# Kernel tuning notes

Hardware: AMD Instinct MI355X
Metric: run time of the kernel (lower is better)

Reference implementation:

```python
import jax, jax.numpy as jnp
import numpy as np

B, T, C = 4, 768, 2048
HEAD_SIZE = 64
H = C // HEAD_SIZE
D_W, D_A, D_MV, D_G = 96, 96, 64, 256
GN_EPS = 1e-5 * 8 ** 2  # head_size_divisor = 8


def _layer_norm(x, w, b, eps=1e-5):
    m = jnp.mean(x, -1, keepdims=True)
    v = jnp.mean(jnp.square(x - m), -1, keepdims=True)
    return (x - m) * jax.lax.rsqrt(v + eps) * w + b


def _time_shift(x):
    # ZeroPad2d((0,0,1,-1)): prepend a zero timestep, drop the last
    return jnp.pad(x, ((0, 0), (1, 0), (0, 0)))[:, :-1]


def _group_norm(x, w, b, eps):
    # x: [M, C], H groups
    M, Cc = x.shape
    xg = x.reshape(M, H, Cc // H)
    m = jnp.mean(xg, -1, keepdims=True)
    v = jnp.mean(jnp.square(xg - m), -1, keepdims=True)
    xg = (xg - m) * jax.lax.rsqrt(v + eps)
    return xg.reshape(M, Cc) * w + b


def _rwkv7(r, w, k, v, a, b):
    # WindBackstepping semantics: S_t = S_{t-1} * diag(exp(-exp(w_t))) + S_{t-1} a_t b_t^T + v_t k_t^T
    # y_t = S_t r_t ; state S is [B,H,N(v),N(k)]
    Bb, Tt, Cc = r.shape
    N = HEAD_SIZE
    r, w, k, v, a, b = [t.reshape(Bb, Tt, H, N) for t in (r, w, k, v, a, b)]
    decay = jnp.exp(-jnp.exp(w))  # [B,T,H,N]
    seq = tuple(jnp.moveaxis(t, 1, 0) for t in (decay, r, k, v, a, b))  # [T,B,H,N]
    s0 = jnp.zeros((Bb, H, N, N), jnp.float32)

    def step(s, inp):
        d_t, r_t, k_t, v_t, a_t, b_t = inp
        sab = jnp.einsum('bhik,bhk,bhj->bhij', s, a_t, b_t)
        s = s * d_t[:, :, None, :] + sab + v_t[..., :, None] * k_t[..., None, :]
        y_t = jnp.einsum('bhij,bhj->bhi', s, r_t)
        return s, y_t

    _, y = jax.lax.scan(step, s0, seq)
    return jnp.moveaxis(y, 0, 1).reshape(Bb, Tt, Cc)


def setup_inputs() -> dict:
    key = jax.random.key(0)
    ks = iter(jax.random.split(key, 48))
    rn = lambda shape, s=1.0: jax.random.normal(next(ks), shape, jnp.float32) * s
    d = {}
    d['x'] = rn((B, T, C))
    d['v_first'] = rn((B, T, C))
    d['ln1_w'] = jnp.ones((C,)); d['ln1_b'] = jnp.zeros((C,))
    d['ln2_w'] = jnp.ones((C,)); d['ln2_b'] = jnp.zeros((C,))
    ddd = jnp.arange(C, dtype=jnp.float32) / C
    for nm, p in [('x_r', 0.2), ('x_w', 0.9), ('x_k', 0.9), ('x_v', 0.4), ('x_a', 0.9), ('x_g', 0.2)]:
        d[nm] = 1.0 - jnp.power(ddd, p)
    d['w0'] = jnp.linspace(-7.0, -2.0, C) + 0.5
    d['w1'] = rn((C, D_W), 0.01); d['w2'] = rn((D_W, C), 0.02)
    d['a0'] = rn((C,), 0.1); d['a1'] = rn((C, D_A), 0.01); d['a2'] = rn((D_A, C), 0.02)
    d['v0'] = 1.0 + rn((C,), 0.1); d['v1'] = rn((C, D_MV), 0.01); d['v2'] = rn((D_MV, C), 0.02)
    d['g1'] = rn((C, D_G), 0.01); d['g2'] = rn((D_G, C), 0.02)
    d['k_k'] = 0.85 * jnp.ones((C,)); d['k_a'] = jnp.ones((C,))
    d['r_k'] = rn((H, HEAD_SIZE), 0.1)
    d['W_r'] = rn((C, C), C ** -0.5)
    d['W_k'] = rn((C, C), C ** -0.5)
    d['W_v'] = rn((C, C), C ** -0.5)
    d['W_o'] = rn((C, C), C ** -0.5)
    d['gn_w'] = jnp.ones((C,)); d['gn_b'] = jnp.zeros((C,))
    d['ffn_x_k'] = 1.0 - ddd
    d['W_key'] = rn((C, 4 * C), C ** -0.5)
    d['W_val'] = rn((4 * C, C), (4 * C) ** -0.5)
    return d


def reference(x, v_first, ln1_w, ln1_b, ln2_w, ln2_b, x_r, x_w, x_k, x_v, x_a, x_g,
              w0, w1, w2, a0, a1, a2, v0, v1, v2, g1, g2, k_k, k_a, r_k,
              W_r, W_k, W_v, W_o, gn_w, gn_b, ffn_x_k, W_key, W_val):
    N = HEAD_SIZE
    # ---- time mix (RWKV_Tmix_x070, layer_id=1) ----
    xn = _layer_norm(x, ln1_w, ln1_b)
    xx = _time_shift(xn) - xn
    xr = xn + xx * x_r
    xw_ = xn + xx * x_w
    xk_ = xn + xx * x_k
    xv_ = xn + xx * x_v
    xa_ = xn + xx * x_a
    xg_ = xn + xx * x_g
    r = xr @ W_r
    w_log = -jax.nn.softplus(-(w0 + jnp.tanh(xw_ @ w1) @ w2)) - 0.5
    k = xk_ @ W_k
    v = xv_ @ W_v
    v = v + (v_first - v) * jax.nn.sigmoid(v0 + (xv_ @ v1) @ v2)  # layer_id != 0
    a = jax.nn.sigmoid(a0 + (xa_ @ a1) @ a2)
    g = jax.nn.sigmoid(xg_ @ g1) @ g2
    kk = (k * k_k).reshape(B, T, H, N)
    kk = kk / jnp.maximum(jnp.linalg.norm(kk, axis=-1, keepdims=True), 1e-12)
    kk = kk.reshape(B, T, C)
    k = k * (1.0 + (a - 1.0) * k_a)
    y = _rwkv7(r, w_log, k, v, -kk, kk * a)
    y = _group_norm(y.reshape(B * T, C), gn_w, gn_b, GN_EPS).reshape(B, T, C)
    rk = jnp.sum(r.reshape(B, T, H, N) * k.reshape(B, T, H, N) * r_k, -1, keepdims=True)
    y = y + (rk * v.reshape(B, T, H, N)).reshape(B, T, C)
    x = x + (y * g) @ W_o
    # ---- channel mix (RWKV_CMix_x070) ----
    x2 = _layer_norm(x, ln2_w, ln2_b)
    xx2 = _time_shift(x2) - x2
    kf = x2 + xx2 * ffn_x_k
    kf = jnp.square(jax.nn.relu(kf @ W_key))
    x = x + kf @ W_val
    return (x, v_first)
```

## Files before the change

kernel.cpp:

```cpp
#include <hip/hip_runtime.h>
#include <stdint.h>

typedef unsigned short u16;
typedef __attribute__((ext_vector_type(8))) short short8;
typedef __attribute__((ext_vector_type(4))) float f32x4;

#define DEVI __device__ __forceinline__

static constexpr int TT = 768;
static constexpr int CC = 2048;
static constexpr int MM = 3072;
static constexpr int HH = 32;

DEVI float b2f(u16 u){ union{float f; unsigned int i;} x; x.i = ((unsigned int)u)<<16; return x.f; }
DEVI float b2fs(short s){ return b2f((u16)s); }
DEVI u16 f2b(float f){
  unsigned int u = __builtin_bit_cast(unsigned int, f);
  unsigned int r = (u + 0x7fffu + ((u>>16)&1u)) >> 16;
  return (u16)r;
}

DEVI void gload16(const void* g, void* s){
  __builtin_amdgcn_global_load_lds((const __attribute__((address_space(1))) void*)g,
                                   (__attribute__((address_space(3))) void*)s, 16, 0, 0);
}

__global__ __launch_bounds__(256) void k_fillf(float* __restrict__ out, float v, int n){
  for (int i = blockIdx.x*256 + threadIdx.x; i < n; i += gridDim.x*256) out[i] = v;
}

__global__ void k_tpose(const float* __restrict__ src, int R, int Cn, u16* __restrict__ dst, int ldd){
  __shared__ float tile[32][33];
  int c0 = blockIdx.x*32, r0 = blockIdx.y*32;
  #pragma unroll
  for (int i=0;i<4;++i){
    int r = r0 + threadIdx.y + i*8, c = c0 + threadIdx.x;
    tile[threadIdx.y + i*8][threadIdx.x] = (r<R && c<Cn) ? src[(size_t)r*Cn + c] : 0.f;
  }
  __syncthreads();
  #pragma unroll
  for (int i=0;i<4;++i){
    int c = c0 + threadIdx.y + i*8, r = r0 + threadIdx.x;
    if (c<Cn && r<R) dst[(size_t)c*ldd + r] = f2b(tile[threadIdx.x][threadIdx.y + i*8]);
  }
}

__global__ __launch_bounds__(256) void k_lnb(const float* __restrict__ in, const float* __restrict__ w,
                                             const float* __restrict__ bias, u16* __restrict__ out){
  __shared__ float red[8];
  int m = blockIdx.x;
  const float* x = in + (size_t)m*CC;
  float v[8]; float s=0.f, ss=0.f;
  #pragma unroll
  for (int i=0;i<8;++i){ v[i] = x[threadIdx.x + i*256]; s += v[i]; ss += v[i]*v[i]; }
  #pragma unroll
  for (int o=32;o;o>>=1){ s += __shfl_xor(s,o); ss += __shfl_xor(ss,o); }
  int wid = threadIdx.x>>6;
  if ((threadIdx.x&63)==0){ red[wid]=s; red[4+wid]=ss; }
  __syncthreads();
  s  = red[0]+red[1]+red[2]+red[3];
  ss = red[4]+red[5]+red[6]+red[7];
  float mean = s*(1.f/2048.f);
  float var  = ss*(1.f/2048.f) - mean*mean;
  float rstd = rsqrtf(fmaxf(var,0.f) + 1e-5f);
  #pragma unroll
  for (int i=0;i<8;++i){
    int c = threadIdx.x + i*256;
    out[(size_t)m*CC + c] = f2b((v[i]-mean)*rstd*w[c] + bias[c]);
  }
}

__global__ __launch_bounds__(256) void k_mixA(const u16* __restrict__ xn,
  const float* __restrict__ cw, const float* __restrict__ ca, const float* __restrict__ cv,
  const float* __restrict__ cg,
  u16* __restrict__ ow, u16* __restrict__ oa, u16* __restrict__ ov, u16* __restrict__ og)
{
  int m = blockIdx.x; int t = m % TT;
  const u16* cur = xn + (size_t)m*CC;
  const u16* prv = cur - CC;
  bool has = (t>0);
  #pragma unroll
  for (int i=0;i<8;++i){
    int c = threadIdx.x + i*256;
    float xc = b2f(cur[c]);
    float xx = (has ? b2f(prv[c]) : 0.f) - xc;
    size_t o = (size_t)m*CC + c;
    ow[o]=f2b(xc + xx*cw[c]); oa[o]=f2b(xc + xx*ca[c]);
    ov[o]=f2b(xc + xx*cv[c]); og[o]=f2b(xc + xx*cg[c]);
  }
}

__global__ __launch_bounds__(256) void k_mixB(const u16* __restrict__ xn,
  const float* __restrict__ cr, const float* __restrict__ ck,
  u16* __restrict__ orr, u16* __restrict__ ok)
{
  int m = blockIdx.x; int t = m % TT;
  const u16* cur = xn + (size_t)m*CC;
  const u16* prv = cur - CC;
  bool has = (t>0);
  #pragma unroll
  for (int i=0;i<8;++i){
    int c = threadIdx.x + i*256;
    float xc = b2f(cur[c]);
    float xx = (has ? b2f(prv[c]) : 0.f) - xc;
    size_t o = (size_t)m*CC + c;
    orr[o]=f2b(xc + xx*cr[c]); ok[o]=f2b(xc + xx*ck[c]);
  }
}

__global__ __launch_bounds__(256) void k_mix1(const u16* __restrict__ xn, const float* __restrict__ cf,
                                              u16* __restrict__ out){
  int m = blockIdx.x; int t = m % TT;
  const u16* cur = xn + (size_t)m*CC;
  const u16* prv = cur - CC;
  bool has = (t>0);
  #pragma unroll
  for (int i=0;i<8;++i){
    int c = threadIdx.x + i*256;
    float xc = b2f(cur[c]);
    float xx = (has ? b2f(prv[c]) : 0.f) - xc;
    out[(size_t)m*CC + c] = f2b(xc + xx*cf[c]);
  }
}

__global__ __launch_bounds__(256,2) void k_gemm(
    const u16* A0, const u16* A1, const u16* A2,
    int amode, int lda,
    const u16* __restrict__ BT, int ldb,
    void* C0, void* C1, void* C2, int ldc, int K,
    int emode, const float* __restrict__ aux)
{
  const int tid = threadIdx.x;
  const int w = tid>>6, l = tid&63;

  const int NT = gridDim.x;
  const int nwg = NT * gridDim.y;
  int bid = blockIdx.y * NT + blockIdx.x;
  int qq = nwg >> 3, rr = nwg & 7;
  int xcd = bid & 7, pos = bid >> 3;
  int nid = (xcd < rr ? xcd*(qq+1) : rr*(qq+1) + (xcd-rr)*qq) + pos;
  const int ntile = nid % NT;
  const int mtile = nid / NT;

  const u16* A = A0;
  if (amode==1){ A = (ntile==0)?A0:(ntile==1)?A1:A2; }
  else if (amode==2){ int g = ntile>>4; A = (g==0)?A0:(g==1)?A1:A2; }

  __shared__ __align__(16) u16 As[3*4096];
  __shared__ __align__(16) u16 Bs[3*4096];

  const int sr = w*16 + (l>>2);
  const int sk = (l&3)*8;
  const u16* Ag = A  + (size_t)(mtile*128 + sr)*lda + sk;
  const u16* Bg = BT + (size_t)(ntile*128 + sr)*ldb + sk;
  const size_t a64 = (size_t)64*lda, b64 = (size_t)64*ldb;
  const int wo = w*512;

  const int wm = w>>1, wn = w&1;
  const int fr = l&15, fk = (l>>4)*8;
  const int aoff = (wm*64 + fr)*32 + fk;
  const int boff = (wn*64 + fr)*32 + fk;

  f32x4 acc[4][4];
  const f32x4 zz = {0.f,0.f,0.f,0.f};
  #pragma unroll
  for (int mi=0;mi<4;++mi)
    #pragma unroll
    for (int ni=0;ni<4;++ni) acc[mi][ni] = zz;

  const int nt = K >> 5;

#define STAGE(bufi, k0) do{ \
    u16* dA = As + (bufi)*4096 + wo; \
    u16* dB = Bs + (bufi)*4096 + wo; \
    gload16(Ag + (k0),        dA); \
    gload16(Ag + a64 + (k0),  dA + 2048); \
    gload16(Bg + (k0),        dB); \
    gload16(Bg + b64 + (k0),  dB + 2048); \
  }while(0)

  STAGE(0, 0);
  if (nt > 1) STAGE(1, 32);

  int cur = 0;
  for (int t=0; t<nt; ++t){
    if (t == nt-1){ asm volatile("s_waitcnt vmcnt(0)" ::: "memory"); }
    else          { asm volatile("s_waitcnt vmcnt(4)" ::: "memory"); }
    __builtin_amdgcn_s_barrier();
    if (t+2 < nt){
      int nb = cur+2; if (nb>=3) nb-=3;
      STAGE(nb, (t+2)<<5);
    }
    const u16* Ab = As + cur*4096;
    const u16* Bb = Bs + cur*4096;
    short8 af[4], bfr[4];
    #pragma unroll
    for (int mi=0;mi<4;++mi) af[mi]  = *(const short8*)(Ab + aoff + mi*512);
    #pragma unroll
    for (int ni=0;ni<4;++ni) bfr[ni] = *(const short8*)(Bb + boff + ni*512);
    #pragma unroll
    for (int mi=0;mi<4;++mi)
      #pragma unroll
      for (int ni=0;ni<4;++ni)
        acc[mi][ni] = __builtin_amdgcn_mfma_f32_16x16x32_bf16(af[mi], bfr[ni], acc[mi][ni], 0,0,0);
    cur = (cur+1==3)?0:cur+1;
  }
#undef STAGE

  const int rb0 = mtile*128 + wm*64 + (l>>4)*4;
  const int cb0 = ntile*128 + wn*64 + fr;
  #pragma unroll
  for (int mi=0;mi<4;++mi){
    #pragma unroll
    for (int ni=0;ni<4;++ni){
      #pragma unroll
      for (int q2=0;q2<4;++q2){
        int row = rb0 + mi*16 + q2;
        int col = cb0 + ni*16;
        float v = acc[mi][ni][q2];
        if (emode==0){
          ((float*)C0)[(size_t)row*ldc + col] = v;
        } else if (emode==1){
          float valw = aux[col] + v;
          float zneg = -valw;
          float sp = (zneg > 20.f) ? zneg : log1pf(expf(zneg));
          float wlog = -sp - 0.5f;
          float dec = expf(-expf(wlog));
          int b_ = row/TT, t_ = row - b_*TT;
          int h_ = col>>6, n_ = col&63;
          ((float*)C0)[((size_t)(b_*HH + h_)*TT + t_)*64 + n_] = dec;
        } else if (emode==2){
          float s = 1.f/(1.f+expf(-(aux[col]+v)));
          ((u16*)C0)[(size_t)row*ldc + col] = f2b(s);
        } else if (emode==3){
          ((float*)C0)[(size_t)row*ldc + col] = aux[(size_t)row*ldc + col] + v;
        } else if (emode==4){
          float r_ = fmaxf(v, 0.f);
          ((u16*)C0)[(size_t)row*ldc + col] = f2b(r_*r_);
        } else if (emode==5){
          ((u16*)C0)[(size_t)row*ldc + col] = f2b(aux[(size_t)row*ldc + col] + v);
        } else if (emode==6){
          ((u16*)C0)[(size_t)row*ldc + col] = f2b(v);
        } else if (emode==7){
          float r_ = v;
          if (col < 128) r_ = tanhf(v);
          else if (col >= 384) r_ = 1.f/(1.f+expf(-v));
          ((u16*)C0)[(size_t)row*ldc + col] = f2b(r_);
        } else if (emode==8){
          int b_ = row/TT, t_ = row - b_*TT;
          int h_ = col>>6, n_ = col&63;
          ((u16*)C0)[((size_t)(b_*HH + h_)*TT + t_)*64 + n_] = f2b(v);
        } else if (emode==9){
          float s = 1.f/(1.f+expf(-(aux[col]+v)));
          int b_ = row/TT, t_ = row - b_*TT;
          int h_ = col>>6, n_ = col&63;
          ((u16*)C0)[((size_t)(b_*HH + h_)*TT + t_)*64 + n_] = f2b(s);
        } else if (emode==10){
          int g = col>>11, c2 = col&2047;
          int b_ = row/TT, t_ = row - b_*TT;
          int h_ = c2>>6, n_ = c2&63;
          u16* dst = (g==0)?(u16*)C0:(g==1)?(u16*)C1:(u16*)C2;
          dst[((size_t)(b_*HH + h_)*TT + t_)*64 + n_] = f2b(v);
        } else {
          float s = 1.f/(1.f+expf(-v));
          ((u16*)C0)[(size_t)row*ldc + (col+384)] = f2b(s);
        }
      }
    }
  }
}

__global__ __launch_bounds__(256) void k_make_rec3(
  u16* __restrict__ ksc, u16* __restrict__ vsc,
  const u16* __restrict__ asc, const u16* __restrict__ gsc,
  float* __restrict__ af, float* __restrict__ bf,
  const float* __restrict__ v_first, const float* __restrict__ k_k, const float* __restrict__ k_a)
{
  int idx = blockIdx.x*4 + (threadIdx.x>>6);
  int l = threadIdx.x & 63;
  int bh = idx / TT, t = idx - bh*TT;
  int b = bh >> 5, h = bh & 31;
  int c = h*64 + l;
  size_t off = (size_t)idx*64 + l;
  size_t mo = ((size_t)b*TT + t)*CC + c;
  float kq = b2f(ksc[off]);
  float vv = b2f(vsc[off]);
  float aa = b2f(asc[off]);
  float sg = b2f(gsc[off]);
  float vf = v_first[mo];
  float kkr = kq * k_k[c];
  float s2 = kkr*kkr;
  #pragma unroll
  for (int o=32;o;o>>=1) s2 += __shfl_xor(s2,o);
  float kk = kkr / fmaxf(sqrtf(s2), 1e-12f);
  ksc[off] = f2b(kq*(1.f + (aa-1.f)*k_a[c]));
  vsc[off] = f2b(vv + (vf-vv)*sg);
  af[off] = -kk;
  bf[off] = kk*aa;
}

static constexpr int RCH = 16;
static constexpr int RNC = TT / RCH;
static constexpr int RBUF = 18432;

__global__ __launch_bounds__(256,1) void k_rwkv(
    const float* __restrict__ decay, const float* __restrict__ af, const float* __restrict__ bf,
    const u16* __restrict__ rb, const u16* __restrict__ kb, const u16* __restrict__ vb,
    u16* __restrict__ y)
{
  __shared__ __align__(16) char lds[3*RBUF];
  int bh = blockIdx.x;
  int b = bh>>5, h = bh&31;
  int tid = threadIdx.x, w = tid>>6, l = tid&63;
  int i = w*16 + (l&15);
  int j0 = (l>>4)*16;
  const size_t base = (size_t)bh * (TT*64);

  const float* dB = decay + base;
  const float* aB = af + base;
  const float* bB = bf + base;
  const u16*  rB = rb + base;
  const u16*  kB = kb + base;
  const u16*  vB = vb + base;

  float S[16];
  #pragma unroll
  for (int q=0;q<16;++q) S[q]=0.f;
  float ycur[RCH], yprev[RCH];
  size_t yb = (size_t)b*TT*CC + h*64 + i;

  const int fe = tid*4;
  const int he = w*256 + l*8;
  const bool hlo = (l < 32);

#define RSTAGE(bufi, c) do{ \
    char* bs = lds + (bufi)*RBUF; \
    size_t cb = (size_t)(c)*1024; \
    gload16(dB + cb + fe, bs + tid*16); \
    gload16(aB + cb + fe, bs + 4096 + tid*16); \
    gload16(bB + cb + fe, bs + 8192 + tid*16); \
    if (hlo){ \
      gload16(rB + cb + he, bs + 12288 + w*512 + l*16); \
      gload16(kB + cb + he, bs + 14336 + w*512 + l*16); \
      gload16(vB + cb + he, bs + 16384 + w*512 + l*16); \
    } \
  }while(0)

  RSTAGE(0, 0);
  RSTAGE(1, 1);

  int cur = 0;
  for (int c=0; c<RNC; ++c){
    if (c == RNC-1){ asm volatile("s_waitcnt vmcnt(0)" ::: "memory"); }
    else           { asm volatile("s_waitcnt vmcnt(6)" ::: "memory"); }
    __builtin_amdgcn_s_barrier();
    if (c > 0){
      int t0 = (c-1)*RCH;
      #pragma unroll
      for (int s=0;s<RCH;++s) y[yb + (size_t)(t0+s)*CC] = f2b(yprev[s]);
    }
    asm volatile("" ::: "memory");
    if (c+2 < RNC){
      int nb = cur+2; if (nb>=3) nb-=3;
      RSTAGE(nb, c+2);
    }
    asm volatile("" ::: "memory");
    const char* bs = lds + cur*RBUF;
    #pragma unroll
    for (int s=0;s<RCH;++s){
      const f32x4* aV = (const f32x4*)(bs + 4096 + s*256 + j0*4);
      float sa = 0.f;
      #pragma unroll
      for (int q=0;q<4;++q){
        f32x4 aq = aV[q];
        #pragma unroll
        for (int e=0;e<4;++e) sa += S[q*4+e]*aq[e];
      }
      sa += __shfl_xor(sa,16); sa += __shfl_xor(sa,32);
      const f32x4* dV = (const f32x4*)(bs + s*256 + j0*4);
      const f32x4* bV = (const f32x4*)(bs + 8192 + s*256 + j0*4);
      const short8* rV = (const short8*)(bs + 12288 + s*128 + j0*2);
      const short8* kV = (const short8*)(bs + 14336 + s*128 + j0*2);
      float vi = b2f(*(const u16*)(bs + 16384 + s*128 + i*2));
      short8 r0 = rV[0], r1 = rV[1];
      short8 k0 = kV[0], k1 = kV[1];
      float yv = 0.f;
      #pragma unroll
      for (int q=0;q<4;++q){
        f32x4 dq = dV[q], bq = bV[q];
        #pragma unroll
        for (int e=0;e<4;++e){
          const int idx = q*4+e;
          float kk = b2fs(idx<8 ? k0[idx] : k1[idx-8]);
          float rr = b2fs(idx<8 ? r0[idx] : r1[idx-8]);
          float Sq = S[idx]*dq[e] + sa*bq[e] + vi*kk;
          S[idx] = Sq;
          yv += Sq*rr;
        }
      }
      yv += __shfl_xor(yv,16); yv += __shfl_xor(yv,32);
      ycur[s] = yv;
    }
    #pragma unroll
    for (int s=0;s<RCH;++s) yprev[s] = ycur[s];
    cur = (cur+1==3)?0:cur+1;
  }
#undef RSTAGE
  {
    int t0 = (RNC-1)*RCH;
    #pragma unroll
    for (int s=0;s<RCH;++s) y[yb + (size_t)(t0+s)*CC] = f2b(yprev[s]);
  }
}

__global__ __launch_bounds__(256) void k_gn(
  const u16* __restrict__ y, const u16* __restrict__ rb, const u16* __restrict__ kb,
  const u16* __restrict__ vb, const float* __restrict__ r_k,
  const float* __restrict__ gnw, const float* __restrict__ gnb,
  const u16* __restrict__ gg, u16* __restrict__ z)
{
  int idx = blockIdx.x*4 + (threadIdx.x>>6);
  int l = threadIdx.x&63;
  int m = idx>>5, h = idx&31;
  int c = h*64 + l;
  size_t mo = (size_t)m*CC + c;
  float yv = b2f(y[mo]);
  float s = yv;
  #pragma unroll
  for (int o=32;o;o>>=1) s += __shfl_xor(s,o);
  float mean = s*(1.f/64.f);
  float dv = yv - mean;
  float vs = dv*dv;
  #pragma unroll
  for (int o=32;o;o>>=1) vs += __shfl_xor(vs,o);
  float gn = dv*rsqrtf(vs*(1.f/64.f) + 6.4e-4f)*gnw[c] + gnb[c];
  size_t ro = ((size_t)((m/TT)*HH + h)*TT + (m%TT))*64 + l;
  float rv=b2f(rb[ro]), kv=b2f(kb[ro]), vv=b2f(vb[ro]);
  float p = rv*kv*r_k[c];
  #pragma unroll
  for (int o=32;o;o>>=1) p += __shfl_xor(p,o);
  z[mo] = f2b((gn + p*vv)*b2f(gg[mo]));
}

extern "C" void kernel_launch(void* const* d_in, const int* in_sizes, int n_in,
                              void* d_out, int out_size, void* d_ws, size_t ws_size,
                              hipStream_t stream)
{
  (void)out_size;
  const float* x      = (const float*)d_in[0];
  const float* v_first= (const float*)d_in[1];
  const float* ln1_w  = (const float*)d_in[2];
  const float* ln1_b  = (const float*)d_in[3];
  const float* ln2_w  = (const float*)d_in[4];
  const float* ln2_b  = (const float*)d_in[5];
  const float* x_r    = (const float*)d_in[6];
  const float* x_w    = (const float*)d_in[7];
  const float* x_k    = (const float*)d_in[8];
  const float* x_v    = (const float*)d_in[9];
  const float* x_a    = (const float*)d_in[10];
  const float* x_g    = (const float*)d_in[11];
  const float* w0     = (const float*)d_in[12];
  const float* w1     = (const float*)d_in[13];
  const float* w2     = (const float*)d_in[14];
  const float* a0     = (const float*)d_in[15];
  const float* a1     = (const float*)d_in[16];
  const float* a2     = (const float*)d_in[17];
  const float* v0     = (const float*)d_in[18];
  const float* v1     = (const float*)d_in[19];
  const float* v2     = (const float*)d_in[20];
  const float* g1     = (const float*)d_in[21];
  const float* g2     = (const float*)d_in[22];
  const float* k_k    = (const float*)d_in[23];
  const float* k_a    = (const float*)d_in[24];
  const float* r_k    = (const float*)d_in[25];
  const float* W_r    = (const float*)d_in[26];
  const float* W_k    = (const float*)d_in[27];
  const float* W_v    = (const float*)d_in[28];
  const float* W_o    = (const float*)d_in[29];
  const float* gn_w   = (const float*)d_in[30];
  const float* gn_b   = (const float*)d_in[31];
  const float* ffn_x_k= (const float*)d_in[32];
  const float* W_key  = (const float*)d_in[33];
  const float* W_val  = (const float*)d_in[34];

  const size_t ME = (size_t)MM*CC;
  float* outF = (float*)d_out;

  bool ok = (n_in==35)
    && in_sizes[0]==6291456 && in_sizes[1]==6291456 && in_sizes[2]==2048
    && in_sizes[12]==2048 && in_sizes[13]==196608 && in_sizes[14]==196608
    && in_sizes[16]==196608 && in_sizes[19]==131072 && in_sizes[21]==524288
    && in_sizes[25]==2048 && in_sizes[26]==4194304 && in_sizes[33]==16777216
    && in_sizes[34]==16777216;
  if (!ok){
    k_fillf<<<2048, 256, 0, stream>>>(outF, 1099511627776.f, (int)ME);
    return;
  }

  constexpr size_t WS_NEED = 125829120 + 12582912;
  if (ws_size < WS_NEED){
    k_fillf<<<2048, 256, 0, stream>>>(outF, (float)(1u<<21) * (float)(ws_size>>20), (int)ME);
    return;
  }
  char* ws = (char*)d_ws;
  float* decay = (float*)(ws + 0);
  float* x1    = (float*)(ws + 0);
  u16* xn   = (u16*)(ws + 25165824);
  u16* WT   = (u16*)(ws + 25165824);
  float* bf32 = (float*)(ws + 25165824);
  u16* xw  = (u16*)(ws + 37748736);
  u16* xr  = (u16*)(ws + 37748736);
  u16* xn2 = (u16*)(ws + 37748736);
  float* af32 = (float*)(ws + 50331648);
  u16* xa  = (u16*)(ws + 50331648);
  u16* xk  = (u16*)(ws + 50331648);
  u16* xv  = (u16*)(ws + 62914560);
  u16* kf  = (u16*)(ws + 62914560);
  u16* xg  = (u16*)(ws + 75497472);
  u16* rsc = (u16*)(ws + 75497472);
  char* Fs = ws + 88080384;
  u16* B1T = (u16*)(Fs);
  u16* w2T = (u16*)(Fs + 2621440);
  u16* a2T = (u16*)(Fs + 3014656);
  u16* v2T = (u16*)(Fs + 3407872);
  u16* g2T = (u16*)(Fs + 3670016);
  u16* H1b = (u16*)(Fs + 4718592);
  u16* ksc = (u16*)(ws + 88080384);
  u16* asc = (u16*)(ws + 100663296);
  u16* ybuf= (u16*)(ws + 100663296);
  u16* gsc = (u16*)(ws + 113246208);
  u16* zbuf= (u16*)(ws + 113246208);
  u16* xcm = (u16*)(ws + 113246208);
  u16* WbigT = (u16*)(ws + 25165824);
  u16* outG = (u16*)(ws + 125829120);
  u16* vsc   = (u16*)d_out;
  u16* WrkvT = ((u16*)d_out) + ME;

  auto GEMM = [&](const u16* a0_, const u16* a1_, const u16* a2_,
                  int amode, int lda_, const u16* bt, int ldb_,
                  void* c0_, void* c1_, void* c2_, int ldc_,
                  int N_, int K_, int em, const float* aux_){
    k_gemm<<<dim3(N_/128, MM/128), 256, 0, stream>>>(a0_,a1_,a2_,amode,lda_,bt,ldb_,c0_,c1_,c2_,ldc_,K_,em,aux_);
  };
  dim3 tb(32,8);

  k_lnb<<<MM, 256, 0, stream>>>(x, ln1_w, ln1_b, xn);
  k_mixA<<<MM, 256, 0, stream>>>(xn, x_w, x_a, x_v, x_g, xw, xa, xv, xg);
  hipMemsetAsync(B1T, 0, 2621440, stream);
  k_tpose<<<dim3(3,64), tb, 0, stream>>>(w1, 2048,  96, B1T + 0*2048,   2048);
  k_tpose<<<dim3(3,64), tb, 0, stream>>>(a1, 2048,  96, B1T + 128*2048, 2048);
  k_tpose<<<dim3(2,64), tb, 0, stream>>>(v1, 2048,  64, B1T + 256*2048, 2048);
  k_tpose<<<dim3(8,64), tb, 0, stream>>>(g1, 2048, 256, B1T + 384*2048, 2048);
  k_tpose<<<dim3(64,3), tb, 0, stream>>>(w2,   96, 2048, w2T,  96);
  k_tpose<<<dim3(64,3), tb, 0, stream>>>(a2,   96, 2048, a2T,  96);
  k_tpose<<<dim3(64,2), tb, 0, stream>>>(v2,   64, 2048, v2T,  64);
  k_tpose<<<dim3(64,8), tb, 0, stream>>>(g2,  256, 2048, g2T, 256);
  GEMM(xw, xa, xv, 1, 2048, B1T, 2048, H1b, nullptr, nullptr, 640, 384, 2048, 7, nullptr);
  GEMM(xg, xg, xg, 0, 2048, B1T + 384*2048, 2048, H1b, nullptr, nullptr, 640, 256, 2048, 11, nullptr);
  GEMM(H1b + 0,   H1b, H1b, 0, 640, w2T,  96, decay, nullptr, nullptr, 2048, 2048,  96, 1, w0);
  GEMM(H1b + 128, H1b, H1b, 0, 640, a2T,  96, asc,   nullptr, nullptr, 2048, 2048,  96, 9, a0);
  GEMM(H1b + 256, H1b, H1b, 0, 640, v2T,  64, gsc,   nullptr, nullptr, 2048, 2048,  64, 9, v0);
  GEMM(H1b + 384, H1b, H1b, 0, 640, g2T, 256, outG,  nullptr, nullptr, 2048, 2048, 256, 6, nullptr);
  k_mixB<<<MM, 256, 0, stream>>>(xn, x_r, x_k, xr, xk);
  k_tpose<<<dim3(64,64), tb, 0, stream>>>(W_r, 2048, 2048, WrkvT,               2048);
  k_tpose<<<dim3(64,64), tb, 0, stream>>>(W_k, 2048, 2048, WrkvT + 2048*2048,   2048);
  k_tpose<<<dim3(64,64), tb, 0, stream>>>(W_v, 2048, 2048, WrkvT + 2*2048*2048, 2048);
  GEMM(xr, xk, xv, 2, 2048, WrkvT, 2048, rsc, ksc, vsc, 2048, 6144, 2048, 10, nullptr);
  k_make_rec3<<<MM*HH/4, 256, 0, stream>>>(ksc, vsc, asc, gsc, af32, bf32, v_first, k_k, k_a);
  k_rwkv<<<128, 256, 0, stream>>>(decay, af32, bf32, rsc, ksc, vsc, ybuf);
  k_gn<<<MM*HH/4, 256, 0, stream>>>(ybuf, rsc, ksc, vsc, r_k, gn_w, gn_b, outG, zbuf);
  k_tpose<<<dim3(64,64), tb, 0, stream>>>(W_o, 2048, 2048, WT, 2048);
  GEMM(zbuf, zbuf, zbuf, 0, 2048, WT, 2048, x1, nullptr, nullptr, 2048, 2048, 2048, 3, x);
  k_lnb<<<MM, 256, 0, stream>>>(x1, ln2_w, ln2_b, xn2);
  k_mix1<<<MM, 256, 0, stream>>>(xn2, ffn_x_k, xcm);
  k_tpose<<<dim3(256,64), tb, 0, stream>>>(W_key, 2048, 8192, WbigT, 2048);
  GEMM(xcm, xcm, xcm, 0, 2048, WbigT, 2048, kf, nullptr, nullptr, 8192, 8192, 2048, 4, nullptr);
  k_tpose<<<dim3(64,256), tb, 0, stream>>>(W_val, 8192, 2048, WbigT, 8192);
  GEMM(kf, kf, kf, 0, 8192, WbigT, 8192, outF, nullptr, nullptr, 2048, 2048, 8192, 3, x1);
  hipMemcpyAsync(outF + ME, v_first, ME*sizeof(float), hipMemcpyDeviceToDevice, stream);
}
```

Measured before the change: 1.551 ms.

## Split RWKV recurrence state rows across two blocks per head

The recurrence kernel now launches two blocks per (batch, head), each owning 32 of the 64 state rows, so each thread holds 8 state elements instead of 16. This doubles the number of active workgroups, from 128 to 256 on a GPU with many CUs, and shortens the per-step dependent arithmetic chain. In exchange, each block still stages the full decay/a/b/r/k/v chunks, which doubles global and LDS traffic. It also adds an extra shuffle-reduction stage per step, and only one lane in eight writes y.

Result: faster. 1.470 ms (-5.2%).

```diff
diff --git a/kernel.cpp b/kernel.cpp
--- a/kernel.cpp
+++ b/kernel.cpp
@@ -309,11 +309,12 @@
     u16* __restrict__ y)
 {
   __shared__ __align__(16) char lds[3*RBUF];
-  int bh = blockIdx.x;
+  int blk = blockIdx.x;
+  int bh = blk >> 1, half = blk & 1;
   int b = bh>>5, h = bh&31;
   int tid = threadIdx.x, w = tid>>6, l = tid&63;
-  int i = w*16 + (l&15);
-  int j0 = (l>>4)*16;
+  const int row = half*32 + w*8 + (l&7);
+  const int j0 = (l>>3)*8;
   const size_t base = (size_t)bh * (TT*64);
 
   const float* dB = decay + base;
@@ -323,11 +324,11 @@
   const u16*  kB = kb + base;
   const u16*  vB = vb + base;
 
-  float S[16];
-  #pragma unroll
-  for (int q=0;q<16;++q) S[q]=0.f;
+  float S[8];
+  #pragma unroll
+  for (int q=0;q<8;++q) S[q]=0.f;
   float ycur[RCH], yprev[RCH];
-  size_t yb = (size_t)b*TT*CC + h*64 + i;
+  size_t yb = (size_t)b*TT*CC + h*64 + row;
 
   const int fe = tid*4;
   const int he = w*256 + l*8;
@@ -357,7 +358,7 @@
     if (c > 0){
       int t0 = (c-1)*RCH;
       #pragma unroll
-      for (int s=0;s<RCH;++s) y[yb + (size_t)(t0+s)*CC] = f2b(yprev[s]);
+      for (int s=0;s<RCH;++s) if (j0==0) y[yb + (size_t)(t0+s)*CC] = f2b(yprev[s]);
     }
     asm volatile("" ::: "memory");
     if (c+2 < RNC){
@@ -369,36 +370,31 @@
     #pragma unroll
     for (int s=0;s<RCH;++s){
       const f32x4* aV = (const f32x4*)(bs + 4096 + s*256 + j0*4);
-      float sa = 0.f;
-      #pragma unroll
-      for (int q=0;q<4;++q){
-        f32x4 aq = aV[q];
-        #pragma unroll
-        for (int e=0;e<4;++e) sa += S[q*4+e]*aq[e];
-      }
-      sa += __shfl_xor(sa,16); sa += __shfl_xor(sa,32);
+      f32x4 a0v = aV[0], a1v = aV[1];
+      float sa = ((S[0]*a0v[0] + S[1]*a0v[1]) + (S[2]*a0v[2] + S[3]*a0v[3]))
+               + ((S[4]*a1v[0] + S[5]*a1v[1]) + (S[6]*a1v[2] + S[7]*a1v[3]));
+      sa += __shfl_xor(sa,8); sa += __shfl_xor(sa,16); sa += __shfl_xor(sa,32);
       const f32x4* dV = (const f32x4*)(bs + s*256 + j0*4);
       const f32x4* bV = (const f32x4*)(bs + 8192 + s*256 + j0*4);
-      const short8* rV = (const short8*)(bs + 12288 + s*128 + j0*2);
-      const short8* kV = (const short8*)(bs + 14336 + s*128 + j0*2);
-      float vi = b2f(*(const u16*)(bs + 16384 + s*128 + i*2));
-      short8 r0 = rV[0], r1 = rV[1];
-      short8 k0 = kV[0], k1 = kV[1];
-      float yv = 0.f;
+      short8 rv8 = *(const short8*)(bs + 12288 + s*128 + j0*2);
+      short8 kv8 = *(const short8*)(bs + 14336 + s*128 + j0*2);
+      float vi = b2f(*(const u16*)(bs + 16384 + s*128 + row*2));
+      f32x4 d0v = dV[0], d1v = dV[1], b0v = bV[0], b1v = bV[1];
+      float y0 = 0.f, y1 = 0.f;
       #pragma unroll
-      for (int q=0;q<4;++q){
-        f32x4 dq = dV[q], bq = bV[q];
-        #pragma unroll
-        for (int e=0;e<4;++e){
-          const int idx = q*4+e;
-          float kk = b2fs(idx<8 ? k0[idx] : k1[idx-8]);
-          float rr = b2fs(idx<8 ? r0[idx] : r1[idx-8]);
-          float Sq = S[idx]*dq[e] + sa*bq[e] + vi*kk;
-          S[idx] = Sq;
-          yv += Sq*rr;
-        }
+      for (int e=0;e<4;++e){
+        float Sq = S[e]*d0v[e] + sa*b0v[e] + vi*b2fs(kv8[e]);
+        S[e] = Sq;
+        y0 += Sq*b2fs(rv8[e]);
       }
-      yv += __shfl_xor(yv,16); yv += __shfl_xor(yv,32);
+      #pragma unroll
+      for (int e=0;e<4;++e){
+        float Sq = S[4+e]*d1v[e] + sa*b1v[e] + vi*b2fs(kv8[4+e]);
+        S[4+e] = Sq;
+        y1 += Sq*b2fs(rv8[4+e]);
+      }
+      float yv = y0 + y1;
+      yv += __shfl_xor(yv,8); yv += __shfl_xor(yv,16); yv += __shfl_xor(yv,32);
       ycur[s] = yv;
     }
     #pragma unroll
@@ -409,7 +405,7 @@
   {
     int t0 = (RNC-1)*RCH;
     #pragma unroll
-    for (int s=0;s<RCH;++s) y[yb + (size_t)(t0+s)*CC] = f2b(yprev[s]);
+    for (int s=0;s<RCH;++s) if (j0==0) y[yb + (size_t)(t0+s)*CC] = f2b(yprev[s]);
   }
 }
 
@@ -567,7 +563,7 @@
   k_tpose<<<dim3(64,64), tb, 0, stream>>>(W_v, 2048, 2048, WrkvT + 2*2048*2048, 2048);
   GEMM(xr, xk, xv, 2, 2048, WrkvT, 2048, rsc, ksc, vsc, 2048, 6144, 2048, 10, nullptr);
   k_make_rec3<<<MM*HH/4, 256, 0, stream>>>(ksc, vsc, asc, gsc, af32, bf32, v_first, k_k, k_a);
-  k_rwkv<<<128, 256, 0, stream>>>(decay, af32, bf32, rsc, ksc, vsc, ybuf);
+  k_rwkv<<<256, 256, 0, stream>>>(decay, af32, bf32, rsc, ksc, vsc, ybuf);
   k_gn<<<MM*HH/4, 256, 0, stream>>>(ybuf, rsc, ksc, vsc, r_k, gn_w, gn_b, outG, zbuf);
   k_tpose<<<dim3(64,64), tb, 0, stream>>>(W_o, 2048, 2048, WT, 2048);
   GEMM(zbuf, zbuf, zbuf, 0, 2048, WT, 2048, x1, nullptr, nullptr, 2048, 2048, 2048, 3, x);
```
